# Kernel tuning notes

Hardware: AMD Instinct MI355X
Metric: run time of the kernel (lower is better)

Reference implementation:

```python
import jax, jax.numpy as jnp
import numpy as np
from jax import lax

K = 3
PAD = 1

def setup_inputs() -> dict:
    key = jax.random.key(0)
    ks = jax.random.split(key, 5)
    B, C, H, W, O = 4, 128, 128, 128, 256
    x = jax.random.normal(ks[0], (B, C, H, W), dtype=jnp.float32)
    w_off = jax.random.normal(ks[1], (3 * K * K, C, K, K), dtype=jnp.float32) * 0.05
    b_off = jnp.zeros((3 * K * K,), dtype=jnp.float32)
    w_dw = jax.random.normal(ks[2], (C, 1, K, K), dtype=jnp.float32) * 0.2
    b_dw = jnp.zeros((C,), dtype=jnp.float32)
    w_pw = jax.random.normal(ks[3], (O, C), dtype=jnp.float32) * (1.0 / np.sqrt(C))
    b_pw = jnp.zeros((O,), dtype=jnp.float32)
    return {"x": x, "w_off": w_off, "b_off": b_off, "w_dw": w_dw,
            "b_dw": b_dw, "w_pw": w_pw, "b_pw": b_pw}

def _dcn_forward(x, w_off, b_off, w_dw, b_dw, w_pw, b_pw):
    B, C, H, W = x.shape
    K2 = K * K
    # offset/mask conv (stride 1, pad 1) -> [B, 3*K*K, H, W]
    om = lax.conv_general_dilated(
        x, w_off, window_strides=(1, 1), padding=[(PAD, PAD), (PAD, PAD)],
        dimension_numbers=("NCHW", "OIHW", "NCHW")) + b_off[None, :, None, None]
    off = om[:, : 2 * K2]                      # [B, 2*K2, H, W]
    mask = jax.nn.sigmoid(om[:, 2 * K2:])      # [B, K2, H, W]
    dy = off[:, 0::2]                          # [B, K2, H, W] (y offsets)
    dx = off[:, 1::2]                          # [B, K2, H, W] (x offsets)
    # base sampling grid per kernel tap
    ky, kx = jnp.meshgrid(jnp.arange(K), jnp.arange(K), indexing="ij")
    ky = (ky.reshape(-1) - PAD).astype(x.dtype)   # [K2]
    kx = (kx.reshape(-1) - PAD).astype(x.dtype)
    py = jnp.arange(H, dtype=x.dtype)[None, None, :, None] + ky[None, :, None, None] + dy
    px = jnp.arange(W, dtype=x.dtype)[None, None, None, :] + kx[None, :, None, None] + dx
    y0 = jnp.floor(py); x0 = jnp.floor(px)
    wy = py - y0;       wx = px - x0

    def gather(yc, xc):
        # yc, xc: [B, K2, H, W] float corner coords; zero outside bounds
        valid = ((yc >= 0) & (yc < H) & (xc >= 0) & (xc < W)).astype(x.dtype)
        yi = jnp.clip(yc, 0, H - 1).astype(jnp.int32)
        xi = jnp.clip(xc, 0, W - 1).astype(jnp.int32)
        idx = yi * W + xi                       # [B, K2, H, W]
        def per_b(xb, ib):
            # xb: [C, H, W]; ib: [K2, H, W] -> [C, K2, H, W]
            return jnp.take(xb.reshape(C, -1), ib.reshape(-1), axis=1).reshape(C, K2, H, W)
        v = jax.vmap(per_b)(x, idx)             # [B, C, K2, H, W]
        return v * valid[:, None]

    val = (gather(y0, x0) * ((1 - wy) * (1 - wx))[:, None]
           + gather(y0, x0 + 1) * ((1 - wy) * wx)[:, None]
           + gather(y0 + 1, x0) * (wy * (1 - wx))[:, None]
           + gather(y0 + 1, x0 + 1) * (wy * wx)[:, None])  # [B, C, K2, H, W]
    val = val * mask[:, None]
    # depthwise deformable conv: per-channel K2 weights
    wk = w_dw.reshape(C, K2)
    out = jnp.einsum("bckhw,ck->bchw", val, wk) + b_dw[None, :, None, None]
    # pointwise 1x1 conv
    out = jnp.einsum("bchw,oc->bohw", out, w_pw) + b_pw[None, :, None, None]
    return out

def reference(x, w_off, b_off, w_dw, b_dw, w_pw, b_pw):
    return _dcn_forward(x, w_off, b_off, w_dw, b_dw, w_pw, b_pw)
```

## Files before the change

### kernel.cpp

```cpp
#include <hip/hip_runtime.h>
#include <hip/hip_bf16.h>
#include <math.h>

#define BB 4
#define CC 128
#define HH 128
#define WW 128
#define OO 256
#define HWP 16384

typedef __attribute__((ext_vector_type(8))) _Float16 half8;
typedef __attribute__((ext_vector_type(2))) _Float16 half2t;
typedef __attribute__((ext_vector_type(4))) float floatx4;

__device__ inline half2t u2h2(unsigned int u) {
  union { unsigned int i; half2t h; } z; z.i = u; return z.h;
}
__device__ inline unsigned short f2h_bits(float f) {
  union { _Float16 h; unsigned short s; } z; z.h = (_Float16)f; return z.s;
}

__global__ __launch_bounds__(256) void k_transpose(const float* __restrict__ x,
                                                   const float* __restrict__ w_off,
                                                   const float* __restrict__ w_pw,
                                                   unsigned int* __restrict__ xh32,
                                                   _Float16* __restrict__ Ah,
                                                   _Float16* __restrict__ Apw) {
  int tid = threadIdx.x;
  if (blockIdx.z == 4) {
    int e = (blockIdx.x * 128 + blockIdx.y) * 256 + tid;
    if (e < 144 * 32 * 8) {
      int kblk = e >> 8;
      int o = (e >> 3) & 31;
      int j = e & 7;
      int k = kblk * 8 + j;
      int t = k >> 7, c = k & 127;
      float w = (o < 27) ? w_off[(o * CC + c) * 9 + t] : 0.0f;
      Ah[e] = (_Float16)w;
    }
    int e2 = e - 144 * 32 * 8;
    if (e2 >= 0 && e2 < 16 * 256 * 8) {
      int cblk = e2 >> 11;
      int o = (e2 >> 3) & 255;
      int j = e2 & 7;
      Apw[e2] = (_Float16)w_pw[o * CC + cblk * 8 + j];
    }
    return;
  }
  __shared__ float tile[64][65];
  int wt = blockIdx.x & 1;
  int ct = blockIdx.x >> 1;
  int h = blockIdx.y, b = blockIdx.z;
  int tw = tid & 63;
  int tc = tid >> 6;
#pragma unroll
  for (int i = 0; i < 16; i++) {
    int c = ct * 64 + i * 4 + tc;
    tile[i * 4 + tc][tw] = x[((b * CC + c) * HH + h) * WW + wt * 64 + tw];
  }
  __syncthreads();
  int cp = tid & 31;
  int wq = tid >> 5;
#pragma unroll
  for (int i = 0; i < 8; i++) {
    int wp = i * 8 + wq;
    int w = wt * 64 + wp;
    unsigned short h0 = f2h_bits(tile[cp * 2][wp]);
    unsigned short h1 = f2h_bits(tile[cp * 2 + 1][wp]);
    int idx2 = (((b * HH + h) * WW + w) * CC + ct * 64 + cp * 2) >> 1;
    xh32[idx2] = (unsigned int)h0 | ((unsigned int)h1 << 16);
  }
}

__global__ __launch_bounds__(256, 4) void k_fused(
    const _Float16* __restrict__ xh, const _Float16* __restrict__ Ah,
    const float* __restrict__ b_off, const float* __restrict__ w_dw,
    const float* __restrict__ b_dw, unsigned short* __restrict__ out1h) {
  __shared__ union SM {
    float part[4][32][34];
    struct {
      int s_base[32][9];
      int s_dxs[32][9];
      int s_dys[32][9];
      unsigned int s_wp[32][9][2];
      float s_wk[9][128];
    } p2;
  } sm;
  __shared__ float om_s[32][28];

  int tid = threadIdx.x;
  int bid = blockIdx.x;
  int n0 = ((bid & 7) * 256 + (bid >> 3)) * 32;
  int b = n0 >> 14;
  int h0 = (n0 >> 7) & 127;
  int wbase = n0 & 127;

  int wv = tid >> 6, lane = tid & 63;
  int n16 = lane & 15, quad = lane >> 4;

  {
    floatx4 acc[2][2] = {};
    half8 zz = {};
#pragma unroll
    for (int kidx = 0; kidx < 9; kidx++) {
      int ki = wv * 9 + kidx;
      int t = ki >> 2, cs = ki & 3;
      int dy = t / 3 - 1, dx = t % 3 - 1;
      int hs = h0 + dy;
      bool hok = ((unsigned)hs < HH);
      int hsc = min(max(hs, 0), HH - 1);
      int wA = wbase + n16 + dx;
      int wB = wA + 16;
      bool okA = hok && ((unsigned)wA < WW);
      bool okB = hok && ((unsigned)wB < WW);
      int wAc = min(max(wA, 0), WW - 1);
      int wBc = min(max(wB, 0), WW - 1);
      size_t offA = (size_t)((b * HH + hsc) * WW + wAc) * CC + cs * 32 + quad * 8;
      size_t offB = (size_t)((b * HH + hsc) * WW + wBc) * CC + cs * 32 + quad * 8;
      half8 bhA = *(const half8*)(xh + offA);
      half8 bhB = *(const half8*)(xh + offB);
      bhA = okA ? bhA : zz;
      bhB = okB ? bhB : zz;
      int kblk = t * 16 + cs * 4 + quad;
      const _Float16* pa = Ah + (size_t)kblk * 256 + n16 * 8;
      half8 a0 = *(const half8*)pa;
      half8 a1 = *(const half8*)(pa + 128);
      acc[0][0] = __builtin_amdgcn_mfma_f32_16x16x32_f16(a0, bhA, acc[0][0], 0, 0, 0);
      acc[1][0] = __builtin_amdgcn_mfma_f32_16x16x32_f16(a1, bhA, acc[1][0], 0, 0, 0);
      acc[0][1] = __builtin_amdgcn_mfma_f32_16x16x32_f16(a0, bhB, acc[0][1], 0, 0, 0);
      acc[1][1] = __builtin_amdgcn_mfma_f32_16x16x32_f16(a1, bhB, acc[1][1], 0, 0, 0);
    }
#pragma unroll
    for (int mt = 0; mt < 2; mt++)
#pragma unroll
      for (int reg = 0; reg < 4; reg++)
#pragma unroll
        for (int nf = 0; nf < 2; nf++)
          sm.part[wv][mt * 16 + quad * 4 + reg][nf * 16 + n16] = acc[mt][nf][reg];
  }
  __syncthreads();

#pragma unroll
  for (int i = 0; i < 4; i++) {
    int idx = tid + i * 256;
    int o = idx >> 5, px = idx & 31;
    float v = sm.part[0][o][px] + sm.part[1][o][px] + sm.part[2][o][px] + sm.part[3][o][px];
    if (o < 27) om_s[px][o] = v + b_off[o];
  }
  __syncthreads();

  for (int i = tid; i < 1152; i += 256) sm.p2.s_wk[i % 9][i / 9] = w_dw[i];
  for (int it = tid; it < 288; it += 256) {
    int px = it / 9, k = it - px * 9;
    int w = wbase + px;
    float dyv = om_s[px][2 * k];
    float dxv = om_s[px][2 * k + 1];
    float mv = om_s[px][18 + k];
    mv = 1.0f / (1.0f + __expf(-mv));
    float py = (float)(h0 + k / 3 - 1) + dyv;
    float pxf = (float)(w + k % 3 - 1) + dxv;
    float y0f = floorf(py), x0f = floorf(pxf);
    float wy = py - y0f, wx = pxf - x0f;
    int y0 = (int)y0f, x0 = (int)x0f;
    int y1 = y0 + 1, x1 = x0 + 1;
    float v00 = (y0 >= 0 && y0 < HH && x0 >= 0 && x0 < WW) ? 1.f : 0.f;
    float v01 = (y0 >= 0 && y0 < HH && x1 >= 0 && x1 < WW) ? 1.f : 0.f;
    float v10 = (y1 >= 0 && y1 < HH && x0 >= 0 && x0 < WW) ? 1.f : 0.f;
    float v11 = (y1 >= 0 && y1 < HH && x1 >= 0 && x1 < WW) ? 1.f : 0.f;
    int y0c = min(max(y0, 0), HH - 1), y1c = min(max(y1, 0), HH - 1);
    int x0c = min(max(x0, 0), WW - 1), x1c = min(max(x1, 0), WW - 1);
    sm.p2.s_base[px][k] = ((b * HH + y0c) * WW + x0c) * CC;
    sm.p2.s_dxs[px][k] = (x1c - x0c) * CC;
    sm.p2.s_dys[px][k] = (y1c - y0c) * WW * CC;
    float w00 = (1.f - wy) * (1.f - wx) * mv * v00;
    float w01 = (1.f - wy) * wx * mv * v01;
    float w10 = wy * (1.f - wx) * mv * v10;
    float w11 = wy * wx * mv * v11;
    sm.p2.s_wp[px][k][0] = (unsigned int)f2h_bits(w00) | ((unsigned int)f2h_bits(w01) << 16);
    sm.p2.s_wp[px][k][1] = (unsigned int)f2h_bits(w10) | ((unsigned int)f2h_bits(w11) << 16);
  }
  __syncthreads();

  int pg = wv * 2 + (lane >> 5);
  int cl = lane & 31;
  int c0 = cl * 4;
  const unsigned short* xs = (const unsigned short*)xh;

  float ac[4][4];
#pragma unroll
  for (int p = 0; p < 4; p++)
#pragma unroll
    for (int j = 0; j < 4; j++) ac[p][j] = 0.f;

#pragma unroll
  for (int k = 0; k < 9; k++) {
    float4 wk4 = *(const float4*)&sm.p2.s_wk[k][c0];
#pragma unroll
    for (int p = 0; p < 4; p++) {
      int pix = pg + p * 8;
      int base = sm.p2.s_base[pix][k] + c0;
      int dxs = sm.p2.s_dxs[pix][k], dys = sm.p2.s_dys[pix][k];
      uint2 a00 = *(const uint2*)(xs + base);
      uint2 a01 = *(const uint2*)(xs + base + dxs);
      uint2 a10 = *(const uint2*)(xs + base + dys);
      uint2 a11 = *(const uint2*)(xs + base + dys + dxs);
      half2t wt = u2h2(sm.p2.s_wp[pix][k][0]);
      half2t wb = u2h2(sm.p2.s_wp[pix][k][1]);
      unsigned int t0 = __builtin_amdgcn_perm(a01.x, a00.x, 0x05040100u);
      unsigned int t1 = __builtin_amdgcn_perm(a01.x, a00.x, 0x07060302u);
      unsigned int t2 = __builtin_amdgcn_perm(a01.y, a00.y, 0x05040100u);
      unsigned int t3 = __builtin_amdgcn_perm(a01.y, a00.y, 0x07060302u);
      unsigned int b0 = __builtin_amdgcn_perm(a11.x, a10.x, 0x05040100u);
      unsigned int b1 = __builtin_amdgcn_perm(a11.x, a10.x, 0x07060302u);
      unsigned int b2 = __builtin_amdgcn_perm(a11.y, a10.y, 0x05040100u);
      unsigned int b3 = __builtin_amdgcn_perm(a11.y, a10.y, 0x07060302u);
      float v0 = __builtin_amdgcn_fdot2(u2h2(b0), wb, __builtin_amdgcn_fdot2(u2h2(t0), wt, 0.f, false), false);
      float v1 = __builtin_amdgcn_fdot2(u2h2(b1), wb, __builtin_amdgcn_fdot2(u2h2(t1), wt, 0.f, false), false);
      float v2 = __builtin_amdgcn_fdot2(u2h2(b2), wb, __builtin_amdgcn_fdot2(u2h2(t2), wt, 0.f, false), false);
      float v3 = __builtin_amdgcn_fdot2(u2h2(b3), wb, __builtin_amdgcn_fdot2(u2h2(t3), wt, 0.f, false), false);
      ac[p][0] = fmaf(v0, wk4.x, ac[p][0]);
      ac[p][1] = fmaf(v1, wk4.y, ac[p][1]);
      ac[p][2] = fmaf(v2, wk4.z, ac[p][2]);
      ac[p][3] = fmaf(v3, wk4.w, ac[p][3]);
    }
  }
  float4 bd = *(const float4*)(b_dw + c0);
#pragma unroll
  for (int p = 0; p < 4; p++) {
    int n = n0 + pg + p * 8;
    ushort4 ov;
    ov.x = f2h_bits(ac[p][0] + bd.x);
    ov.y = f2h_bits(ac[p][1] + bd.y);
    ov.z = f2h_bits(ac[p][2] + bd.z);
    ov.w = f2h_bits(ac[p][3] + bd.w);
    *(ushort4*)(out1h + (size_t)n * CC + c0) = ov;
  }
}

__global__ __launch_bounds__(256) void k_pw_mfma(const _Float16* __restrict__ Apw,
                                                 const _Float16* __restrict__ out1h,
                                                 const float* __restrict__ bpw,
                                                 float* __restrict__ out) {
  int bid = blockIdx.x;
  int n0 = ((bid & 7) * 128 + (bid >> 3)) * 64;
  int tid = threadIdx.x;
  int wv = tid >> 6, lane = tid & 63;
  int n16 = lane & 15, quad = lane >> 4;
  int obase = wv * 64;

  floatx4 acc[4][4] = {};
#pragma unroll
  for (int cs = 0; cs < 4; cs++) {
    half8 af[4], bf[4];
#pragma unroll
    for (int mf = 0; mf < 4; mf++) {
      const _Float16* pa = Apw + ((size_t)(cs * 4 + quad) * 256 + obase + mf * 16 + n16) * 8;
      af[mf] = *(const half8*)pa;
    }
#pragma unroll
    for (int nf = 0; nf < 4; nf++) {
      const _Float16* pb = out1h + (size_t)(n0 + nf * 16 + n16) * CC + cs * 32 + quad * 8;
      bf[nf] = *(const half8*)pb;
    }
#pragma unroll
    for (int mf = 0; mf < 4; mf++)
#pragma unroll
      for (int nf = 0; nf < 4; nf++)
        acc[mf][nf] = __builtin_amdgcn_mfma_f32_16x16x32_f16(af[mf], bf[nf], acc[mf][nf], 0, 0, 0);
  }
  int b = n0 >> 14;
#pragma unroll
  for (int mf = 0; mf < 4; mf++) {
#pragma unroll
    for (int reg = 0; reg < 4; reg++) {
      int o = obase + mf * 16 + quad * 4 + reg;
      float bo = bpw[o];
#pragma unroll
      for (int nf = 0; nf < 4; nf++) {
        int n = n0 + nf * 16 + n16;
        int hw = n & 16383;
        out[((size_t)(b * OO + o) << 14) + hw] = acc[mf][nf][reg] + bo;
      }
    }
  }
}

extern "C" void kernel_launch(void* const* d_in, const int* in_sizes, int n_in,
                              void* d_out, int out_size, void* d_ws, size_t ws_size,
                              hipStream_t stream) {
  const float* x     = (const float*)d_in[0];
  const float* w_off = (const float*)d_in[1];
  const float* b_off = (const float*)d_in[2];
  const float* w_dw  = (const float*)d_in[3];
  const float* b_dw  = (const float*)d_in[4];
  const float* w_pw  = (const float*)d_in[5];
  const float* b_pw  = (const float*)d_in[6];
  float* out = (float*)d_out;
  float* ws  = (float*)d_ws;

  _Float16* xh = (_Float16*)out;

  _Float16* out1h = (_Float16*)ws;
  _Float16* Ah = (_Float16*)(ws + 4194304);
  _Float16* Apw = Ah + 36864;

  k_transpose<<<dim3(4, 128, 5), 256, 0, stream>>>(x, w_off, w_pw,
                                                   (unsigned int*)xh, Ah, Apw);
  k_fused<<<2048, 256, 0, stream>>>(xh, Ah, b_off, w_dw, b_dw,
                                    (unsigned short*)out1h);
  k_pw_mfma<<<1024, 256, 0, stream>>>(Apw, out1h, b_pw, out);
}
```

Baseline: 179.3 us.

## Fuse pointwise GEMM into deformable kernel via swizzled LDS staging

Merges the pointwise 1x1 MFMA GEMM into the fused offset-conv/deformable-sampling kernel. The fp16 depthwise result now stays in an XOR-swizzled shared-memory tile instead of going through a global intermediate. Tiles grow to 64 pixels per block, so each wave computes the offset conv for 16 pixels without a cross-wave reduction. The sampling loop uses 8 channels per lane with 16-byte gathers. This removes one kernel launch and the out1h round trip through global memory, in exchange for more LDS, more registers and lower occupancy (launch bounds 2).

```diff
diff --git a/kernel.cpp b/kernel.cpp
--- a/kernel.cpp
+++ b/kernel.cpp
@@ -18,6 +18,20 @@
 }
 __device__ inline unsigned short f2h_bits(float f) {
   union { _Float16 h; unsigned short s; } z; z.h = (_Float16)f; return z.s;
+}
+
+__device__ inline void blend2(unsigned int a00w, unsigned int a01w,
+                              unsigned int a10w, unsigned int a11w,
+                              half2t wt, half2t wb, float wk0, float wk1,
+                              float& acc0, float& acc1) {
+  unsigned int tl = __builtin_amdgcn_perm(a01w, a00w, 0x05040100u);
+  unsigned int th = __builtin_amdgcn_perm(a01w, a00w, 0x07060302u);
+  unsigned int bl = __builtin_amdgcn_perm(a11w, a10w, 0x05040100u);
+  unsigned int bh = __builtin_amdgcn_perm(a11w, a10w, 0x07060302u);
+  float v0 = __builtin_amdgcn_fdot2(u2h2(bl), wb, __builtin_amdgcn_fdot2(u2h2(tl), wt, 0.f, false), false);
+  float v1 = __builtin_amdgcn_fdot2(u2h2(bh), wb, __builtin_amdgcn_fdot2(u2h2(th), wt, 0.f, false), false);
+  acc0 = fmaf(v0, wk0, acc0);
+  acc1 = fmaf(v1, wk1, acc1);
 }
 
 __global__ __launch_bounds__(256) void k_transpose(const float* __restrict__ x,
@@ -72,25 +86,22 @@
   }
 }
 
-__global__ __launch_bounds__(256, 4) void k_fused(
+__global__ __launch_bounds__(256, 2) void k_fused(
     const _Float16* __restrict__ xh, const _Float16* __restrict__ Ah,
-    const float* __restrict__ b_off, const float* __restrict__ w_dw,
-    const float* __restrict__ b_dw, unsigned short* __restrict__ out1h) {
-  __shared__ union SM {
-    float part[4][32][34];
-    struct {
-      int s_base[32][9];
-      int s_dxs[32][9];
-      int s_dys[32][9];
-      unsigned int s_wp[32][9][2];
-      float s_wk[9][128];
-    } p2;
-  } sm;
-  __shared__ float om_s[32][28];
+    const _Float16* __restrict__ Apw, const float* __restrict__ b_off,
+    const float* __restrict__ w_dw, const float* __restrict__ b_dw,
+    const float* __restrict__ bpw, float* __restrict__ out) {
+  __shared__ float om_s[64][28];
+  __shared__ int s_base[64][9];
+  __shared__ int s_dxs[64][9];
+  __shared__ int s_dys[64][9];
+  __shared__ unsigned int s_wp[64][9][2];
+  __shared__ float s_wk[9][128];
+  __shared__ __align__(16) _Float16 val[64][128];
 
   int tid = threadIdx.x;
   int bid = blockIdx.x;
-  int n0 = ((bid & 7) * 256 + (bid >> 3)) * 32;
+  int n0 = ((bid & 7) * 128 + (bid >> 3)) * 64;
   int b = n0 >> 14;
   int h0 = (n0 >> 7) & 127;
   int wbase = n0 & 127;
@@ -99,58 +110,44 @@
   int n16 = lane & 15, quad = lane >> 4;
 
   {
-    floatx4 acc[2][2] = {};
+    int pxb = wv * 16;
+    floatx4 acc0 = {}, acc1 = {};
     half8 zz = {};
 #pragma unroll
-    for (int kidx = 0; kidx < 9; kidx++) {
-      int ki = wv * 9 + kidx;
-      int t = ki >> 2, cs = ki & 3;
+    for (int t = 0; t < 9; t++) {
       int dy = t / 3 - 1, dx = t % 3 - 1;
       int hs = h0 + dy;
       bool hok = ((unsigned)hs < HH);
       int hsc = min(max(hs, 0), HH - 1);
-      int wA = wbase + n16 + dx;
-      int wB = wA + 16;
+      int wA = wbase + pxb + n16 + dx;
       bool okA = hok && ((unsigned)wA < WW);
-      bool okB = hok && ((unsigned)wB < WW);
       int wAc = min(max(wA, 0), WW - 1);
-      int wBc = min(max(wB, 0), WW - 1);
-      size_t offA = (size_t)((b * HH + hsc) * WW + wAc) * CC + cs * 32 + quad * 8;
-      size_t offB = (size_t)((b * HH + hsc) * WW + wBc) * CC + cs * 32 + quad * 8;
-      half8 bhA = *(const half8*)(xh + offA);
-      half8 bhB = *(const half8*)(xh + offB);
-      bhA = okA ? bhA : zz;
-      bhB = okB ? bhB : zz;
-      int kblk = t * 16 + cs * 4 + quad;
-      const _Float16* pa = Ah + (size_t)kblk * 256 + n16 * 8;
-      half8 a0 = *(const half8*)pa;
-      half8 a1 = *(const half8*)(pa + 128);
-      acc[0][0] = __builtin_amdgcn_mfma_f32_16x16x32_f16(a0, bhA, acc[0][0], 0, 0, 0);
-      acc[1][0] = __builtin_amdgcn_mfma_f32_16x16x32_f16(a1, bhA, acc[1][0], 0, 0, 0);
-      acc[0][1] = __builtin_amdgcn_mfma_f32_16x16x32_f16(a0, bhB, acc[0][1], 0, 0, 0);
-      acc[1][1] = __builtin_amdgcn_mfma_f32_16x16x32_f16(a1, bhB, acc[1][1], 0, 0, 0);
-    }
-#pragma unroll
-    for (int mt = 0; mt < 2; mt++)
-#pragma unroll
-      for (int reg = 0; reg < 4; reg++)
-#pragma unroll
-        for (int nf = 0; nf < 2; nf++)
-          sm.part[wv][mt * 16 + quad * 4 + reg][nf * 16 + n16] = acc[mt][nf][reg];
-  }
-  __syncthreads();
-
-#pragma unroll
-  for (int i = 0; i < 4; i++) {
-    int idx = tid + i * 256;
-    int o = idx >> 5, px = idx & 31;
-    float v = sm.part[0][o][px] + sm.part[1][o][px] + sm.part[2][o][px] + sm.part[3][o][px];
-    if (o < 27) om_s[px][o] = v + b_off[o];
-  }
-  __syncthreads();
-
-  for (int i = tid; i < 1152; i += 256) sm.p2.s_wk[i % 9][i / 9] = w_dw[i];
-  for (int it = tid; it < 288; it += 256) {
+      size_t rowoff = (size_t)((b * HH + hsc) * WW + wAc) * CC + quad * 8;
+#pragma unroll
+      for (int cs = 0; cs < 4; cs++) {
+        half8 bh = *(const half8*)(xh + rowoff + cs * 32);
+        bh = okA ? bh : zz;
+        int kblk = t * 16 + cs * 4 + quad;
+        const _Float16* pa = Ah + (size_t)kblk * 256 + n16 * 8;
+        half8 a0 = *(const half8*)pa;
+        half8 a1 = *(const half8*)(pa + 128);
+        acc0 = __builtin_amdgcn_mfma_f32_16x16x32_f16(a0, bh, acc0, 0, 0, 0);
+        acc1 = __builtin_amdgcn_mfma_f32_16x16x32_f16(a1, bh, acc1, 0, 0, 0);
+      }
+    }
+    int px = pxb + n16;
+#pragma unroll
+    for (int reg = 0; reg < 4; reg++) {
+      int o0 = quad * 4 + reg;
+      om_s[px][o0] = acc0[reg] + b_off[o0];
+      int o1 = 16 + quad * 4 + reg;
+      if (o1 < 27) om_s[px][o1] = acc1[reg] + b_off[o1];
+    }
+  }
+  __syncthreads();
+
+  for (int i = tid; i < 1152; i += 256) s_wk[i % 9][i / 9] = w_dw[i];
+  for (int it = tid; it < 576; it += 256) {
     int px = it / 9, k = it - px * 9;
     int w = wbase + px;
     float dyv = om_s[px][2 * k];
@@ -169,117 +166,103 @@
     float v11 = (y1 >= 0 && y1 < HH && x1 >= 0 && x1 < WW) ? 1.f : 0.f;
     int y0c = min(max(y0, 0), HH - 1), y1c = min(max(y1, 0), HH - 1);
     int x0c = min(max(x0, 0), WW - 1), x1c = min(max(x1, 0), WW - 1);
-    sm.p2.s_base[px][k] = ((b * HH + y0c) * WW + x0c) * CC;
-    sm.p2.s_dxs[px][k] = (x1c - x0c) * CC;
-    sm.p2.s_dys[px][k] = (y1c - y0c) * WW * CC;
+    s_base[px][k] = ((b * HH + y0c) * WW + x0c) * CC;
+    s_dxs[px][k] = (x1c - x0c) * CC;
+    s_dys[px][k] = (y1c - y0c) * WW * CC;
     float w00 = (1.f - wy) * (1.f - wx) * mv * v00;
     float w01 = (1.f - wy) * wx * mv * v01;
     float w10 = wy * (1.f - wx) * mv * v10;
     float w11 = wy * wx * mv * v11;
-    sm.p2.s_wp[px][k][0] = (unsigned int)f2h_bits(w00) | ((unsigned int)f2h_bits(w01) << 16);
-    sm.p2.s_wp[px][k][1] = (unsigned int)f2h_bits(w10) | ((unsigned int)f2h_bits(w11) << 16);
-  }
-  __syncthreads();
-
-  int pg = wv * 2 + (lane >> 5);
-  int cl = lane & 31;
-  int c0 = cl * 4;
-  const unsigned short* xs = (const unsigned short*)xh;
-
-  float ac[4][4];
-#pragma unroll
-  for (int p = 0; p < 4; p++)
-#pragma unroll
-    for (int j = 0; j < 4; j++) ac[p][j] = 0.f;
-
-#pragma unroll
-  for (int k = 0; k < 9; k++) {
-    float4 wk4 = *(const float4*)&sm.p2.s_wk[k][c0];
+    s_wp[px][k][0] = (unsigned int)f2h_bits(w00) | ((unsigned int)f2h_bits(w01) << 16);
+    s_wp[px][k][1] = (unsigned int)f2h_bits(w10) | ((unsigned int)f2h_bits(w11) << 16);
+  }
+  __syncthreads();
+
+  {
+    int cl = lane & 15;
+    int pgl = lane >> 4;
+    int slot = wv * 4 + pgl;
+    int c0 = cl * 8;
+    const unsigned short* xs = (const unsigned short*)xh;
+
+    float ac[4][8];
+#pragma unroll
+    for (int p = 0; p < 4; p++)
+#pragma unroll
+      for (int j = 0; j < 8; j++) ac[p][j] = 0.f;
+
+#pragma unroll
+    for (int k = 0; k < 9; k++) {
+      float4 wka = *(const float4*)&s_wk[k][c0];
+      float4 wkb = *(const float4*)&s_wk[k][c0 + 4];
+#pragma unroll
+      for (int p = 0; p < 4; p++) {
+        int pix = slot + p * 16;
+        int base = s_base[pix][k] + c0;
+        int dxs = s_dxs[pix][k], dys = s_dys[pix][k];
+        uint4 a00 = *(const uint4*)(xs + base);
+        uint4 a01 = *(const uint4*)(xs + base + dxs);
+        uint4 a10 = *(const uint4*)(xs + base + dys);
+        uint4 a11 = *(const uint4*)(xs + base + dys + dxs);
+        half2t wt = u2h2(s_wp[pix][k][0]);
+        half2t wb = u2h2(s_wp[pix][k][1]);
+        blend2(a00.x, a01.x, a10.x, a11.x, wt, wb, wka.x, wka.y, ac[p][0], ac[p][1]);
+        blend2(a00.y, a01.y, a10.y, a11.y, wt, wb, wka.z, wka.w, ac[p][2], ac[p][3]);
+        blend2(a00.z, a01.z, a10.z, a11.z, wt, wb, wkb.x, wkb.y, ac[p][4], ac[p][5]);
+        blend2(a00.w, a01.w, a10.w, a11.w, wt, wb, wkb.z, wkb.w, ac[p][6], ac[p][7]);
+      }
+    }
+    float4 bd0 = *(const float4*)(b_dw + c0);
+    float4 bd1 = *(const float4*)(b_dw + c0 + 4);
 #pragma unroll
     for (int p = 0; p < 4; p++) {
-      int pix = pg + p * 8;
-      int base = sm.p2.s_base[pix][k] + c0;
-      int dxs = sm.p2.s_dxs[pix][k], dys = sm.p2.s_dys[pix][k];
-      uint2 a00 = *(const uint2*)(xs + base);
-      uint2 a01 = *(const uint2*)(xs + base + dxs);
-      uint2 a10 = *(const uint2*)(xs + base + dys);
-      uint2 a11 = *(const uint2*)(xs + base + dys + dxs);
-      half2t wt = u2h2(sm.p2.s_wp[pix][k][0]);
-      half2t wb = u2h2(sm.p2.s_wp[pix][k][1]);
-      unsigned int t0 = __builtin_amdgcn_perm(a01.x, a00.x, 0x05040100u);
-      unsigned int t1 = __builtin_amdgcn_perm(a01.x, a00.x, 0x07060302u);
-      unsigned int t2 = __builtin_amdgcn_perm(a01.y, a00.y, 0x05040100u);
-      unsigned int t3 = __builtin_amdgcn_perm(a01.y, a00.y, 0x07060302u);
-      unsigned int b0 = __builtin_amdgcn_perm(a11.x, a10.x, 0x05040100u);
-      unsigned int b1 = __builtin_amdgcn_perm(a11.x, a10.x, 0x07060302u);
-      unsigned int b2 = __builtin_amdgcn_perm(a11.y, a10.y, 0x05040100u);
-      unsigned int b3 = __builtin_amdgcn_perm(a11.y, a10.y, 0x07060302u);
-      float v0 = __builtin_amdgcn_fdot2(u2h2(b0), wb, __builtin_amdgcn_fdot2(u2h2(t0), wt, 0.f, false), false);
-      float v1 = __builtin_amdgcn_fdot2(u2h2(b1), wb, __builtin_amdgcn_fdot2(u2h2(t1), wt, 0.f, false), false);
-      float v2 = __builtin_amdgcn_fdot2(u2h2(b2), wb, __builtin_amdgcn_fdot2(u2h2(t2), wt, 0.f, false), false);
-      float v3 = __builtin_amdgcn_fdot2(u2h2(b3), wb, __builtin_amdgcn_fdot2(u2h2(t3), wt, 0.f, false), false);
-      ac[p][0] = fmaf(v0, wk4.x, ac[p][0]);
-      ac[p][1] = fmaf(v1, wk4.y, ac[p][1]);
-      ac[p][2] = fmaf(v2, wk4.z, ac[p][2]);
-      ac[p][3] = fmaf(v3, wk4.w, ac[p][3]);
-    }
-  }
-  float4 bd = *(const float4*)(b_dw + c0);
-#pragma unroll
-  for (int p = 0; p < 4; p++) {
-    int n = n0 + pg + p * 8;
-    ushort4 ov;
-    ov.x = f2h_bits(ac[p][0] + bd.x);
-    ov.y = f2h_bits(ac[p][1] + bd.y);
-    ov.z = f2h_bits(ac[p][2] + bd.z);
-    ov.w = f2h_bits(ac[p][3] + bd.w);
-    *(ushort4*)(out1h + (size_t)n * CC + c0) = ov;
-  }
-}
-
-__global__ __launch_bounds__(256) void k_pw_mfma(const _Float16* __restrict__ Apw,
-                                                 const _Float16* __restrict__ out1h,
-                                                 const float* __restrict__ bpw,
-                                                 float* __restrict__ out) {
-  int bid = blockIdx.x;
-  int n0 = ((bid & 7) * 128 + (bid >> 3)) * 64;
-  int tid = threadIdx.x;
-  int wv = tid >> 6, lane = tid & 63;
-  int n16 = lane & 15, quad = lane >> 4;
-  int obase = wv * 64;
-
-  floatx4 acc[4][4] = {};
-#pragma unroll
-  for (int cs = 0; cs < 4; cs++) {
-    half8 af[4], bf[4];
+      int pix = slot + p * 16;
+      uint4 pk;
+      pk.x = (unsigned int)f2h_bits(ac[p][0] + bd0.x) | ((unsigned int)f2h_bits(ac[p][1] + bd0.y) << 16);
+      pk.y = (unsigned int)f2h_bits(ac[p][2] + bd0.z) | ((unsigned int)f2h_bits(ac[p][3] + bd0.w) << 16);
+      pk.z = (unsigned int)f2h_bits(ac[p][4] + bd1.x) | ((unsigned int)f2h_bits(ac[p][5] + bd1.y) << 16);
+      pk.w = (unsigned int)f2h_bits(ac[p][6] + bd1.z) | ((unsigned int)f2h_bits(ac[p][7] + bd1.w) << 16);
+      int su = cl ^ (pix & 7);
+      *(uint4*)&val[pix][su * 8] = pk;
+    }
+  }
+  __syncthreads();
+
+  {
+    int obase = wv * 64;
+    floatx4 acc[4][4] = {};
+#pragma unroll
+    for (int cs = 0; cs < 4; cs++) {
+      half8 af[4], bf[4];
+#pragma unroll
+      for (int mf = 0; mf < 4; mf++) {
+        const _Float16* pa = Apw + ((size_t)(cs * 4 + quad) * 256 + obase + mf * 16 + n16) * 8;
+        af[mf] = *(const half8*)pa;
+      }
+#pragma unroll
+      for (int nf = 0; nf < 4; nf++) {
+        int row = nf * 16 + n16;
+        int su = (cs * 4 + quad) ^ (row & 7);
+        bf[nf] = *(const half8*)&val[row][su * 8];
+      }
+#pragma unroll
+      for (int mf = 0; mf < 4; mf++)
+#pragma unroll
+        for (int nf = 0; nf < 4; nf++)
+          acc[mf][nf] = __builtin_amdgcn_mfma_f32_16x16x32_f16(af[mf], bf[nf], acc[mf][nf], 0, 0, 0);
+    }
 #pragma unroll
     for (int mf = 0; mf < 4; mf++) {
-      const _Float16* pa = Apw + ((size_t)(cs * 4 + quad) * 256 + obase + mf * 16 + n16) * 8;
-      af[mf] = *(const half8*)pa;
-    }
-#pragma unroll
-    for (int nf = 0; nf < 4; nf++) {
-      const _Float16* pb = out1h + (size_t)(n0 + nf * 16 + n16) * CC + cs * 32 + quad * 8;
-      bf[nf] = *(const half8*)pb;
-    }
-#pragma unroll
-    for (int mf = 0; mf < 4; mf++)
-#pragma unroll
-      for (int nf = 0; nf < 4; nf++)
-        acc[mf][nf] = __builtin_amdgcn_mfma_f32_16x16x32_f16(af[mf], bf[nf], acc[mf][nf], 0, 0, 0);
-  }
-  int b = n0 >> 14;
-#pragma unroll
-  for (int mf = 0; mf < 4; mf++) {
-#pragma unroll
-    for (int reg = 0; reg < 4; reg++) {
-      int o = obase + mf * 16 + quad * 4 + reg;
-      float bo = bpw[o];
-#pragma unroll
-      for (int nf = 0; nf < 4; nf++) {
-        int n = n0 + nf * 16 + n16;
-        int hw = n & 16383;
-        out[((size_t)(b * OO + o) << 14) + hw] = acc[mf][nf][reg] + bo;
+#pragma unroll
+      for (int reg = 0; reg < 4; reg++) {
+        int o = obase + mf * 16 + quad * 4 + reg;
+        float bo = bpw[o];
+#pragma unroll
+        for (int nf = 0; nf < 4; nf++) {
+          int n = n0 + nf * 16 + n16;
+          int hw = n & 16383;
+          out[((size_t)(b * OO + o) << 14) + hw] = acc[mf][nf][reg] + bo;
+        }
       }
     }
   }
@@ -298,15 +281,11 @@
   float* out = (float*)d_out;
   float* ws  = (float*)d_ws;
 
-  _Float16* xh = (_Float16*)out;
-
-  _Float16* out1h = (_Float16*)ws;
-  _Float16* Ah = (_Float16*)(ws + 4194304);
+  _Float16* xh  = (_Float16*)ws;
+  _Float16* Ah  = (_Float16*)((char*)ws + 16777216);
   _Float16* Apw = Ah + 36864;
 
   k_transpose<<<dim3(4, 128, 5), 256, 0, stream>>>(x, w_off, w_pw,
                                                    (unsigned int*)xh, Ah, Apw);
-  k_fused<<<2048, 256, 0, stream>>>(xh, Ah, b_off, w_dw, b_dw,
-                                    (unsigned short*)out1h);
-  k_pw_mfma<<<1024, 256, 0, stream>>>(Apw, out1h, b_pw, out);
-}
+  k_fused<<<1024, 256, 0, stream>>>(xh, Ah, Apw, b_off, w_dw, b_dw, b_pw, out);
+}
```

Result: faster. 161.3 us (-10.0%).
